# Optimization experiments

Measured on AMD Instinct MI355X. Metric: run time of the kernel, lower is better.

Reference implementation:

```python
import jax, jax.numpy as jnp
import numpy as np
from functools import partial

# Config (BranchNet 'big'-style)
HIST = [42, 78, 150, 294, 582]
PW = [3, 6, 12, 24, 48]
SHIFTING = [False, False, True, True, True]
CW = 7          # conv width
F = 32          # conv filters
E = 32          # embedding dims
B = 4096        # batch
H_TOT = 590     # total history length
V = 8192        # 2**(pc_hash_bits+1)
WBITS = 2       # weight quantization bits
ABITS = 3       # activation quantization bits
EPS = 1e-5


@partial(jax.custom_vjp, nondiff_argnums=(1,))
def quant_signed(x, bits):
    # Quantize.forward (signed, bits>1): round(x*scale)/scale, scale=(1<<(bits-1))-1
    scale = float((1 << (bits - 1)) - 1)
    return jnp.round(x * scale) / scale

def _q_fwd(x, bits):
    return quant_signed(x, bits), None

def _q_bwd(bits, res, g):
    # straight-through estimator, matching Quantize.backward
    return (g,)

quant_signed.defvjp(_q_fwd, _q_bwd)


def batchnorm(x, gamma, beta, axes, pshape):
    # training-mode BatchNorm1d: batch statistics, biased variance
    m = jnp.mean(x, axis=axes, keepdims=True)
    v = jnp.var(x, axis=axes, keepdims=True)
    return gamma.reshape(pshape) * (x - m) * jax.lax.rsqrt(v + EPS) + beta.reshape(pshape)


def extract_slice_history(x, global_shift, slice_size, pooling_width, shifting):
    # vectorized version of the per-sample Python loop in extract_slice_history
    h_tot = x.shape[1]
    if shifting:
        s = jnp.mod(global_shift, pooling_width)              # [B]
        start = (h_tot - s - slice_size)[:, None]             # [B,1]
        idx = start + jnp.arange(slice_size)[None, :]         # [B,L]
        return jnp.take_along_axis(x, idx, axis=1)
    return x[:, -slice_size:]


def fc_layer(x, W, b, gamma, beta):
    # FCLayer with quantized weights + batchnorm + hardtanh + quantized act
    w = quant_signed(jnp.clip(W, -1.0, 1.0), WBITS)
    y = x @ w.T + b
    y = batchnorm(y, gamma, beta, (0,), (1, -1))
    y = jnp.clip(y, -1.0, 1.0)  # hardtanh
    return quant_signed(y, ABITS)


def branchnet_forward(x, global_shift, emb, conv_w, conv_b, bn1_g, bn1_b,
                      bnp_g, bnp_b, W1, b1, g1, be1, W2, b2, g2, be2, W3, b3):
    feats = []
    for i in range(len(HIST)):
        L, pw = HIST[i], PW[i]
        xs = extract_slice_history(x, global_shift, L, pw, SHIFTING[i])  # [B,L] int
        e = jnp.take(emb[i], xs, axis=0)                                 # [B,L,E]
        e = jnp.transpose(e, (0, 2, 1))                                  # [B,E,L]
        h = jax.lax.conv_general_dilated(
            e, conv_w[i], window_strides=(1,), padding='VALID',
            dimension_numbers=('NCH', 'OIH', 'NCH')) + conv_b[i][None, :, None]
        h = batchnorm(h, bn1_g[i], bn1_b[i], (0, 2), (1, -1, 1))
        h = jnp.tanh(h)
        T = (L - CW + 1) // pw                                           # = 12
        p = h[:, :, :T * pw].reshape(h.shape[0], F, T, pw).mean(axis=-1) # AvgPool1d
        p = batchnorm(p, bnp_g[i], bnp_b[i], (0, 2), (1, -1, 1))
        feats.append(p.reshape(p.shape[0], -1))                          # [B, F*T]
    z = jnp.concatenate(feats, axis=1)                                   # [B, 1920]
    z = fc_layer(z, W1, b1, g1, be1)
    z = fc_layer(z, W2, b2, g2, be2)
    w3 = quant_signed(jnp.clip(W3, -1.0, 1.0), WBITS)
    out = z @ w3.T + b3                                                  # [B,1]
    return out[:, 0]                                                     # squeeze(dim=1)


def setup_inputs() -> dict:
    key = jax.random.key(0)
    ks = jax.random.split(key, 12)
    return {
        'x': jax.random.randint(ks[0], (B, H_TOT), 0, V, dtype=jnp.int32),
        'global_shift': jax.random.randint(ks[1], (B,), 0, 48, dtype=jnp.int32),
        'emb': jax.random.normal(ks[2], (5, V, E), jnp.float32) * 0.1,
        'conv_w': jax.random.normal(ks[3], (5, F, E, CW), jnp.float32) * 0.1,
        'conv_b': jax.random.normal(ks[4], (5, F), jnp.float32) * 0.01,
        'bn1_g': jnp.ones((5, F), jnp.float32),
        'bn1_b': jnp.zeros((5, F), jnp.float32),
        'bnp_g': jnp.ones((5, F), jnp.float32),
        'bnp_b': jnp.zeros((5, F), jnp.float32),
        'W1': jax.random.uniform(ks[5], (2048, 1920), jnp.float32, -1.0, 1.0),
        'b1': jax.random.normal(ks[6], (2048,), jnp.float32) * 0.01,
        'g1': jnp.ones((2048,), jnp.float32),
        'be1': jnp.zeros((2048,), jnp.float32),
        'W2': jax.random.uniform(ks[7], (2048, 2048), jnp.float32, -1.0, 1.0),
        'b2': jax.random.normal(ks[8], (2048,), jnp.float32) * 0.01,
        'g2': jnp.ones((2048,), jnp.float32),
        'be2': jnp.zeros((2048,), jnp.float32),
        'W3': jax.random.uniform(ks[9], (1, 2048), jnp.float32, -1.0, 1.0),
        'b3': jax.random.normal(ks[10], (1,), jnp.float32) * 0.01,
    }


def reference(x, global_shift, emb, conv_w, conv_b, bn1_g, bn1_b, bnp_g, bnp_b,
              W1, b1, g1, be1, W2, b2, g2, be2, W3, b3):
    return branchnet_forward(x, global_shift, emb, conv_w, conv_b, bn1_g, bn1_b,
                             bnp_g, bnp_b, W1, b1, g1, be1, W2, b2, g2, be2, W3, b3)
```

## Files before the change

kernel.cpp:

```cpp
#include <hip/hip_runtime.h>
#include <cmath>

#define HTOT  590
#define BATCH 4096
#define VOCAB 8192

typedef _Float16 f16;
typedef __attribute__((ext_vector_type(8))) _Float16 f16x8;
typedef __attribute__((ext_vector_type(4))) _Float16 f16x4;
typedef __attribute__((ext_vector_type(4))) float f32x4;
typedef __attribute__((ext_vector_type(16))) float f32x16;

constexpr size_t OFF_EHL  = 0;
constexpr size_t OFF_WF   = 1310720;
constexpr size_t OFF_PA   = 1347584;
constexpr size_t OFF_PB   = 2921472;
constexpr size_t OFF_BN1  = 4494336;
constexpr size_t OFF_BNP  = 4494656;
constexpr size_t OFF_CP   = 4494976;
constexpr size_t OFF_BNF1 = 4626048;
constexpr size_t OFF_PRAW = 4630528;
constexpr size_t OFF_W1P  = 12494848;
constexpr size_t OFF_W2P  = 14460928;
constexpr size_t OFF_Y    = 16558080;
constexpr size_t OFF_BNF2 = 24946688;
constexpr size_t OFF_Z2K  = 0;
constexpr size_t OFF_Z3K  = 4194304;

__device__ __forceinline__ float qw(float w) {
  return rintf(fminf(fmaxf(w, -1.f), 1.f));
}
__device__ __forceinline__ float4 ld4(const float* p) {
  return *reinterpret_cast<const float4*>(p);
}
__device__ __forceinline__ float tanh_c(float u) {
  const float e = __expf(2.f*u);
  return 1.f - __fdividef(2.f, e + 1.f);
}

#define MF(A,B,C) __builtin_amdgcn_mfma_f32_32x32x16_f16(A,B,C,0,0,0)

__global__ __launch_bounds__(256) void k_eprep(const float* __restrict__ emb,
                                               f16* __restrict__ ehl)
{
  const int idx = blockIdx.x*256 + threadIdx.x;
  const int c = idx & 31, v = (idx >> 5) & 8191, slice = idx >> 18;
  const float val = emb[(size_t)(slice*VOCAB + v)*32 + c];
  const f16 hi = (f16)val;
  const f16 lo = (f16)((val - (float)hi)*2048.f);
  f16* row = ehl + (size_t)(slice*VOCAB + v)*64;
  row[c] = hi; row[32 + c] = lo;
}

__global__ __launch_bounds__(256) void k_wfprep(const float* __restrict__ convw,
                                                f16* __restrict__ wf)
{
  const int idx = blockIdx.x*256 + threadIdx.x;
  const int j = idx & 7, lane = (idx >> 3) & 63, hl = (idx >> 9) & 1, ks = (idx >> 10) & 1;
  const int kk = idx >> 11, k = kk % 7, slice = kk / 7;
  const int f = lane & 31, c = ks*16 + (lane >> 5)*8 + j;
  const float val = convw[((slice*32 + f)*32 + c)*7 + k];
  const f16 hi = (f16)val;
  wf[idx] = hl ? (f16)((val - (float)hi)*2048.f) : hi;
}

template<int PASS>
__global__ __launch_bounds__(256, 2) void k_convm(const int* __restrict__ x,
                                                  const int* __restrict__ gshift,
                                                  const float* __restrict__ ehl,
                                                  const float* __restrict__ wfrag,
                                                  const float* __restrict__ bn1,
                                                  float* __restrict__ z,
                                                  float* __restrict__ partials)
{
  const int b = blockIdx.x;
  const int type = blockIdx.y;
  const int tid = threadIdx.x;
  const int wid = tid >> 6, lane = tid & 63;
  const int lt = lane & 31, hf = lane >> 5;

  __shared__ float smem[10584];
  __shared__ int   tokid[294];
  __shared__ float stat[(PASS==0)?256:4];

  float* tokrow = smem;
  float* thbuf  = smem;
  float* poolb  = smem + 4224;

  const int gsv = gshift[b];
  const int NTOK = (type == 0) ? 270 : 294;

  for (int i = tid; i < NTOK; i += 256) {
    int xs, q = i;
    if (type == 0) {
      if (i < 42)       { xs = 548; }
      else if (i < 120) { xs = 512; q = i - 42; }
      else              { xs = 440 - gsv % 12; q = i - 120; }
    } else if (type == 1) xs = 296 - gsv % 24;
    else if (type == 2)   xs = 8 - gsv % 48;
    else                  xs = 8 - gsv % 48 + 288;
    int xi = xs + q; if (xi < 0) xi += HTOT;
    tokid[i] = x[b*HTOT + xi];
  }
  __syncthreads();

  for (int j = tid; j < NTOK*8; j += 256) {
    const int row = j >> 3, ch = j & 7;
    const int sl = (type == 0) ? (row < 42 ? 0 : (row < 120 ? 1 : 2)) : ((type == 1) ? 3 : 4);
    const float4 v = ld4(ehl + (size_t)(sl*VOCAB + tokid[row])*32 + ch*4);
    *reinterpret_cast<float4*>(&tokrow[row*36 + ch*4]) = v;
  }
  __syncthreads();

  int slice, tb, nt, slotoff, ThV, pw, si;
  if (type == 0) {
    if      (wid == 0) { slice=0; tb=0;  nt=2; slotoff=0;   ThV=36;  pw=3;  si=0; }
    else if (wid == 1) { slice=1; tb=0;  nt=3; slotoff=42;  ThV=72;  pw=6;  si=1; }
    else if (wid == 2) { slice=2; tb=0;  nt=3; slotoff=120; ThV=144; pw=12; si=2; }
    else               { slice=2; tb=96; nt=2; slotoff=120; ThV=144; pw=12; si=2; }
  } else if (type == 1) {
    slice=3; pw=24; ThV=288; slotoff=0; si=0;
    tb = (wid == 0) ? 0 : 32 + wid*64; nt = (wid == 0) ? 3 : 2;
  } else if (type == 2) {
    slice=4; pw=48; ThV=288; slotoff=0; si=0;
    tb = (wid == 0) ? 0 : 32 + wid*64; nt = (wid == 0) ? 3 : 2;
  } else {
    slice=4; pw=48; ThV=576; slotoff=-288; si=0;
    tb = 288 + ((wid == 0) ? 0 : 32 + wid*64); nt = (wid == 0) ? 3 : 2;
  }
  const int wb = (type == 3) ? 6 : 0;

  const float* wfsl = wfrag + slice*7168;
  #define LDA(K,KS,HL) (*reinterpret_cast<const f16x8*>(wfsl + (((K)*2+(KS))*2+(HL))*256 + lane*4))

  f32x16 a0[3], a1[3];
  #pragma unroll
  for (int r = 0; r < 3; ++r) {
    #pragma unroll
    for (int i = 0; i < 16; ++i) { a0[r][i] = 0.f; a1[r][i] = 0.f; }
  }

  const float* p0 = tokrow + (size_t)(slotoff + tb + lt)*36 + hf*4;
  const float* p1 = p0 + 1152;
  const float* p2 = p0 + 2304;
  f16x8 wh0 = LDA(0,0,0), wl0 = LDA(0,0,1), wh1 = LDA(0,1,0), wl1 = LDA(0,1,1);
  #pragma unroll 1
  for (int k = 0; k < 7; ++k) {
    f16x8 nh0, nl0, nh1, nl1;
    if (k < 6) { nh0 = LDA(k+1,0,0); nl0 = LDA(k+1,0,1); nh1 = LDA(k+1,1,0); nl1 = LDA(k+1,1,1); }
    {
      const f16x8 bh0 = *(const f16x8*)(p0),    bh1 = *(const f16x8*)(p0+8);
      const f16x8 bl0 = *(const f16x8*)(p0+16), bl1 = *(const f16x8*)(p0+24);
      a0[0]=MF(wh0,bh0,a0[0]); a1[0]=MF(wh0,bl0,a1[0]); a1[0]=MF(wl0,bh0,a1[0]);
      a0[0]=MF(wh1,bh1,a0[0]); a1[0]=MF(wh1,bl1,a1[0]); a1[0]=MF(wl1,bh1,a1[0]);
    }
    if (nt > 1) {
      const f16x8 bh0 = *(const f16x8*)(p1),    bh1 = *(const f16x8*)(p1+8);
      const f16x8 bl0 = *(const f16x8*)(p1+16), bl1 = *(const f16x8*)(p1+24);
      a0[1]=MF(wh0,bh0,a0[1]); a1[1]=MF(wh0,bl0,a1[1]); a1[1]=MF(wl0,bh0,a1[1]);
      a0[1]=MF(wh1,bh1,a0[1]); a1[1]=MF(wh1,bl1,a1[1]); a1[1]=MF(wl1,bh1,a1[1]);
    }
    if (nt > 2) {
      const f16x8 bh0 = *(const f16x8*)(p2),    bh1 = *(const f16x8*)(p2+8);
      const f16x8 bl0 = *(const f16x8*)(p2+16), bl1 = *(const f16x8*)(p2+24);
      a0[2]=MF(wh0,bh0,a0[2]); a1[2]=MF(wh0,bl0,a1[2]); a1[2]=MF(wl0,bh0,a1[2]);
      a0[2]=MF(wh1,bh1,a0[2]); a1[2]=MF(wh1,bl1,a1[2]); a1[2]=MF(wl1,bh1,a1[2]);
    }
    p0 += 36; p1 += 36; p2 += 36;
    wh0 = nh0; wl0 = nl0; wh1 = nh1; wl1 = nl1;
  }
  __syncthreads();

  if (PASS == 1) {
    for (int i = tid; i < 2304; i += 256) poolb[i] = 0.f;
  }
  __syncthreads();

  float sv1[16], sv2[16], A1v[16], B1v[16];
  if (PASS == 0) {
    #pragma unroll
    for (int i = 0; i < 16; ++i) { sv1[i] = 0.f; sv2[i] = 0.f; }
  } else {
    #pragma unroll
    for (int i = 0; i < 16; ++i) {
      const int fr = (i&3) + 8*(i>>2) + 4*hf;
      A1v[i] = bn1[slice*32 + fr];
      B1v[i] = bn1[160 + slice*32 + fr];
    }
  }

  #pragma unroll
  for (int r = 0; r < 3; ++r) if (r < nt) {
    const int tbg = tb + r*32;
    float h[16];
    #pragma unroll
    for (int i = 0; i < 16; ++i) h[i] = a0[r][i] + a1[r][i]*(1.f/2048.f);
    if (PASS == 0) {
      const bool tv = (tbg + lt) < ThV;
      #pragma unroll
      for (int i = 0; i < 16; ++i) {
        const float hv = tv ? h[i] : 0.f;
        sv1[i] += hv; sv2[i] += hv*hv;
      }
    } else {
      #pragma unroll
      for (int i = 0; i < 16; ++i) {
        const int fr = (i&3) + 8*(i>>2) + 4*hf;
        thbuf[wid*1056 + fr*33 + lt] = tanh_c(A1v[i]*h[i] + B1v[i]);
      }
      const int tvend = min(tbg + 32, ThV);
      const int wlo = tbg / pw, whi = (tvend - 1) / pw;
      for (int w = wlo; w <= whi; ++w) {
        const int lo = max(w*pw, tbg), hi2 = min((w+1)*pw, tvend);
        float s = 0.f;
        for (int t = lo + hf; t < hi2; t += 2) s += thbuf[wid*1056 + lt*33 + (t - tbg)];
        s += __shfl_xor(s, 32);
        if (hf == 0) {
          const int piece = (w*pw < tbg) ? 1 : 0;
          poolb[(si*12 + (w - wb))*64 + piece*32 + lt] = s;
        }
      }
    }
  }

  if (PASS == 0) {
    #pragma unroll
    for (int i = 0; i < 16; ++i) {
      #pragma unroll
      for (int m = 1; m < 32; m <<= 1) {
        sv1[i] += __shfl_xor(sv1[i], m, 32);
        sv2[i] += __shfl_xor(sv2[i], m, 32);
      }
    }
    if (lt == 0) {
      #pragma unroll
      for (int i = 0; i < 16; ++i) {
        stat[wid*64 + hf*32 + i*2]     = sv1[i];
        stat[wid*64 + hf*32 + i*2 + 1] = sv2[i];
      }
    }
  }
  __syncthreads();

  const int nch = (type == 0) ? 96 : 32;
  if (tid < nch) {
    const int sic = tid >> 5, f = tid & 31;
    const int sg = (type == 0) ? sic : ((type == 1) ? 3 : 4);
    const int P = (sg < 4) ? sg*32 + f : ((type == 2) ? 128 + f : 160 + f);
    float s1 = 0.f, s2 = 0.f;
    if (PASS == 0) {
      const int hfc = (f >> 2) & 1, ic = (f & 3) + 4*(f >> 3);
      #pragma unroll
      for (int w = 0; w < 4; ++w) {
        const int wsi = (type == 0) ? ((w < 2) ? w : 2) : 0;
        if (wsi == sic) {
          s1 += stat[w*64 + hfc*32 + ic*2];
          s2 += stat[w*64 + hfc*32 + ic*2 + 1];
        }
      }
    } else {
      const int pwc = (type == 0) ? ((sic == 0) ? 3 : (sic == 1) ? 6 : 12)
                                  : ((type == 1) ? 24 : 48);
      const int nwin = (type >= 2) ? 6 : 12;
      const int wbc = (type == 3) ? 6 : 0;
      const float inv = 1.f/(float)pwc;
      for (int wl = 0; wl < nwin; ++wl) {
        const float p = (poolb[(sic*12 + wl)*64 + f] + poolb[(sic*12 + wl)*64 + 32 + f]) * inv;
        z[(size_t)b*1920 + sg*384 + (wl + wbc)*32 + f] = p;
        s1 += p; s2 += p*p;
      }
    }
    partials[(size_t)b*384 + P*2]     = s1;
    partials[(size_t)b*384 + P*2 + 1] = s2;
  }
}

template<int PASS>
__global__ __launch_bounds__(256) void k_bnfinal(const float* __restrict__ partials,
                                                 const float* __restrict__ gamma,
                                                 const float* __restrict__ beta,
                                                 float* __restrict__ outAB)
{
  const int c = blockIdx.x;
  const int slice = c >> 5, f = c & 31;
  const int tid = threadIdx.x;
  double s1 = 0.0, s2 = 0.0;
  for (int b = tid; b < BATCH; b += 256) {
    const float* p = partials + (size_t)b*384;
    if (slice < 4) { s1 += p[(slice*32+f)*2]; s2 += p[(slice*32+f)*2+1]; }
    else {
      s1 += (double)p[(128+f)*2]   + (double)p[(160+f)*2];
      s2 += (double)p[(128+f)*2+1] + (double)p[(160+f)*2+1];
    }
  }
  __shared__ double r1[256], r2[256];
  r1[tid] = s1; r2[tid] = s2;
  __syncthreads();
  for (int off = 128; off > 0; off >>= 1) {
    if (tid < off) { r1[tid] += r1[tid+off]; r2[tid] += r2[tid+off]; }
    __syncthreads();
  }
  if (tid == 0) {
    long N;
    if (PASS == 0) { const long Tall[5] = {36,72,144,288,576}; N = (long)BATCH * Tall[slice]; }
    else           { N = (long)BATCH * 12; }
    const double m   = r1[0]/(double)N;
    const double var = r2[0]/(double)N - m*m;
    const float rstd = (float)(1.0/sqrt(var + 1e-5));
    const float Aa = gamma[c]*rstd;
    outAB[c]       = Aa;
    outAB[160 + c] = beta[c] - Aa*(float)m;
  }
}

__global__ __launch_bounds__(256) void k_znorm(float* __restrict__ zz,
                                               const float* __restrict__ bnp)
{
  const size_t i4 = (size_t)blockIdx.x*256 + threadIdx.x;
  const float4 v = ld4(zz + i4*4);
  const int j = (int)((i4*4) % 1920);
  const int slice = j / 384, f0 = j & 31;
  const float4 A = ld4(bnp + slice*32 + f0);
  const float4 B = ld4(bnp + 160 + slice*32 + f0);
  const float zn[4] = {v.x*A.x+B.x, v.y*A.y+B.y, v.z*A.z+B.z, v.w*A.w+B.w};
  uint4 pk;
  unsigned w[4];
  #pragma unroll
  for (int e = 0; e < 4; ++e) {
    const f16 hi = (f16)zn[e];
    const f16 lo = (f16)(zn[e] - (float)hi);
    w[e] = (unsigned)__builtin_bit_cast(unsigned short, hi)
         | ((unsigned)__builtin_bit_cast(unsigned short, lo) << 16);
  }
  pk.x = w[0]; pk.y = w[1]; pk.z = w[2]; pk.w = w[3];
  *reinterpret_cast<uint4*>(zz + i4*4) = pk;
}

__global__ __launch_bounds__(256) void k_wprep1(const float* __restrict__ W1,
                                                f16* __restrict__ W1p)
{
  const int idx = blockIdx.x*256 + threadIdx.x;
  const int n = idx / 1920, klds = idx - n*1920;
  const int slice = klds / 384, r = klds - slice*384;
  const int tp = r >> 5, f = r & 31;
  W1p[idx] = (f16)qw(W1[n*1920 + slice*384 + f*12 + tp]);
}

__global__ __launch_bounds__(256) void k_wprep2(const float* __restrict__ W2,
                                                f16* __restrict__ W2p)
{
  const size_t i4 = (size_t)blockIdx.x*256 + threadIdx.x;
  const float4 v = ld4(W2 + i4*4);
  f16x4 o;
  o[0] = (f16)qw(v.x); o[1] = (f16)qw(v.y); o[2] = (f16)qw(v.z); o[3] = (f16)qw(v.w);
  *reinterpret_cast<f16x4*>(&W2p[i4*4]) = o;
}

template<int SPLIT, int PACKED>
__global__ __launch_bounds__(256) void k_mfgemm(const f16* __restrict__ Ahi,
                                               const unsigned* __restrict__ Apk,
                                               const f16* __restrict__ Bp,
                                               float* __restrict__ C,
                                               const int K, const float oscale)
{
  __shared__ f16 sA[(SPLIT+1)*128][40];
  __shared__ f16 sB[128][40];
  const int tid = threadIdx.x;
  const int bm = blockIdx.y*128, bn = blockIdx.x*128;
  const int wid = tid >> 6, lane = tid & 63;
  const int wm = (wid >> 1)*64, wn = (wid & 1)*64;
  const int lgrp = lane >> 4, lrow = lane & 15;
  f32x4 acc[4][4];
  #pragma unroll
  for (int m = 0; m < 4; ++m)
    #pragma unroll
    for (int n = 0; n < 4; ++n) acc[m][n] = (f32x4){0.f,0.f,0.f,0.f};

  const int srow = tid >> 2, sc = (tid & 3)*8;
  for (int k0 = 0; k0 < K; k0 += 32) {
    #pragma unroll
    for (int u = 0; u < 2; ++u) {
      const int row = srow + u*64;
      if (PACKED) {
        const unsigned* ap = Apk + (size_t)(bm+row)*K + k0 + sc;
        const uint4 v0 = *reinterpret_cast<const uint4*>(ap);
        const uint4 v1 = *reinterpret_cast<const uint4*>(ap + 4);
        uint4 hi, lo;
        hi.x = (v0.x & 0xffffu) | (v0.y << 16);  hi.y = (v0.z & 0xffffu) | (v0.w << 16);
        hi.z = (v1.x & 0xffffu) | (v1.y << 16);  hi.w = (v1.z & 0xffffu) | (v1.w << 16);
        lo.x = (v0.x >> 16) | (v0.y & 0xffff0000u);  lo.y = (v0.z >> 16) | (v0.w & 0xffff0000u);
        lo.z = (v1.x >> 16) | (v1.y & 0xffff0000u);  lo.w = (v1.z >> 16) | (v1.w & 0xffff0000u);
        *reinterpret_cast<uint4*>(&sA[row][sc])     = hi;
        *reinterpret_cast<uint4*>(&sA[128+row][sc]) = lo;
      } else {
        const uint4 va = *reinterpret_cast<const uint4*>(&Ahi[(size_t)(bm+row)*K + k0 + sc]);
        *reinterpret_cast<uint4*>(&sA[row][sc]) = va;
      }
      const uint4 vb = *reinterpret_cast<const uint4*>(&Bp[(size_t)(bn+row)*K + k0 + sc]);
      *reinterpret_cast<uint4*>(&sB[row][sc]) = vb;
    }
    __syncthreads();
    f16x8 bf[4];
    #pragma unroll
    for (int n = 0; n < 4; ++n)
      bf[n] = *reinterpret_cast<const f16x8*>(&sB[wn + n*16 + lrow][lgrp*8]);
    #pragma unroll
    for (int m = 0; m < 4; ++m) {
      const f16x8 ah = *reinterpret_cast<const f16x8*>(&sA[wm + m*16 + lrow][lgrp*8]);
      #pragma unroll
      for (int n = 0; n < 4; ++n)
        acc[m][n] = __builtin_amdgcn_mfma_f32_16x16x32_f16(ah, bf[n], acc[m][n], 0, 0, 0);
      if (SPLIT) {
        const f16x8 al = *reinterpret_cast<const f16x8*>(&sA[128 + wm + m*16 + lrow][lgrp*8]);
        #pragma unroll
        for (int n = 0; n < 4; ++n)
          acc[m][n] = __builtin_amdgcn_mfma_f32_16x16x32_f16(al, bf[n], acc[m][n], 0, 0, 0);
      }
    }
    __syncthreads();
  }
  #pragma unroll
  for (int m = 0; m < 4; ++m)
    #pragma unroll
    for (int n = 0; n < 4; ++n) {
      const int col = bn + wn + n*16 + lrow;
      #pragma unroll
      for (int r = 0; r < 4; ++r)
        C[(size_t)(bm + wm + m*16 + lgrp*4 + r)*2048 + col] = acc[m][n][r]*oscale;
    }
}

__global__ __launch_bounds__(256) void k_colpart(const float* __restrict__ Y,
                                                 double* __restrict__ part, int N)
{
  const int c0 = blockIdx.x*64;
  const int chunk = blockIdx.y;
  const int tid = threadIdx.x;
  const int c = tid & 63, rq = tid >> 6;
  double s1 = 0.0, s2 = 0.0;
  const int rbase = chunk*256;
  for (int r = rbase + rq; r < rbase+256; r += 4) {
    const float v = Y[(size_t)r*N + c0 + c];
    s1 += (double)v; s2 += (double)v*(double)v;
  }
  __shared__ double r1[256], r2[256];
  r1[tid] = s1; r2[tid] = s2;
  __syncthreads();
  if (tid < 64) {
    const double a  = r1[tid]+r1[tid+64]+r1[tid+128]+r1[tid+192];
    const double cc = r2[tid]+r2[tid+64]+r2[tid+128]+r2[tid+192];
    part[(size_t)(c0+c)*32 + chunk*2]     = a;
    part[(size_t)(c0+c)*32 + chunk*2 + 1] = cc;
  }
}

__global__ __launch_bounds__(256) void k_colfinal(const double* __restrict__ part,
                                                  const float* __restrict__ gamma,
                                                  const float* __restrict__ beta,
                                                  float* __restrict__ bnfc, int N)
{
  const int c = blockIdx.x*256 + threadIdx.x;
  if (c >= N) return;
  double s1 = 0.0, s2 = 0.0;
  #pragma unroll
  for (int ch = 0; ch < 16; ++ch) {
    s1 += part[(size_t)c*32 + ch*2];
    s2 += part[(size_t)c*32 + ch*2 + 1];
  }
  const double m   = s1/4096.0;
  const double var = s2/4096.0 - m*m;
  const float rstd = (float)(1.0/sqrt(var + 1e-5));
  const float Aa = gamma[c]*rstd;
  bnfc[c]        = Aa;
  bnfc[2048 + c] = beta[c] - Aa*(float)m;
}

__global__ __launch_bounds__(256) void k_act(const float* __restrict__ Y,
                                             const float* __restrict__ bnfc,
                                             f16* __restrict__ Zk)
{
  const size_t i4 = (size_t)blockIdx.x*256 + threadIdx.x;
  const int cbase = (int)((i4*4) & 2047);
  const float4 v = ld4(Y + i4*4);
  const float4 A = ld4(bnfc + cbase);
  const float4 B = ld4(bnfc + 2048 + cbase);
  const float t[4] = {v.x*A.x+B.x, v.y*A.y+B.y, v.z*A.z+B.z, v.w*A.w+B.w};
  f16x4 o;
  #pragma unroll
  for (int e = 0; e < 4; ++e) {
    const float c = fminf(fmaxf(t[e], -1.f), 1.f);
    o[e] = (f16)rintf(c*3.f);
  }
  *reinterpret_cast<f16x4*>(&Zk[i4*4]) = o;
}

__global__ __launch_bounds__(256) void k_final(const f16* __restrict__ Z3,
                                               const float* __restrict__ W3,
                                               const float* __restrict__ b3,
                                               float* __restrict__ out)
{
  const int b = blockIdx.x;
  const int tid = threadIdx.x;
  float s = 0.f;
  for (int j = tid; j < 2048; j += 256)
    s += (float)Z3[(size_t)b*2048 + j] * qw(W3[j]);
  __shared__ float red[256];
  red[tid] = s;
  __syncthreads();
  for (int off = 128; off > 0; off >>= 1) {
    if (tid < off) red[tid] += red[tid+off];
    __syncthreads();
  }
  if (tid == 0) out[b] = red[0]*(1.f/3.f) + b3[0];
}

extern "C" void kernel_launch(void* const* d_in, const int* in_sizes, int n_in,
                              void* d_out, int out_size, void* d_ws, size_t ws_size,
                              hipStream_t stream)
{
  const int*   x    = (const int*)d_in[0];
  const int*   gs   = (const int*)d_in[1];
  const float* emb  = (const float*)d_in[2];
  const float* cw   = (const float*)d_in[3];
  const float* bn1g = (const float*)d_in[5];
  const float* bn1b = (const float*)d_in[6];
  const float* bnpg = (const float*)d_in[7];
  const float* bnpb = (const float*)d_in[8];
  const float* W1   = (const float*)d_in[9];
  const float* g1   = (const float*)d_in[11];
  const float* be1  = (const float*)d_in[12];
  const float* W2   = (const float*)d_in[13];
  const float* g2   = (const float*)d_in[15];
  const float* be2  = (const float*)d_in[16];
  const float* W3   = (const float*)d_in[17];
  const float* b3   = (const float*)d_in[18];
  float* ws  = (float*)d_ws;
  float* out = (float*)d_out;

  k_eprep<<<5120, 256, 0, stream>>>(emb, (f16*)(ws + OFF_EHL));
  k_wfprep<<<280, 256, 0, stream>>>(cw, (f16*)(ws + OFF_WF));

  k_convm<0><<<dim3(BATCH, 4), 256, 0, stream>>>(x, gs, ws + OFF_EHL, ws + OFF_WF,
                                                 ws + OFF_BN1, nullptr, ws + OFF_PA);
  k_bnfinal<0><<<160, 256, 0, stream>>>(ws + OFF_PA, bn1g, bn1b, ws + OFF_BN1);
  k_convm<1><<<dim3(BATCH, 4), 256, 0, stream>>>(x, gs, ws + OFF_EHL, ws + OFF_WF,
                                                 ws + OFF_BN1, ws + OFF_PRAW, ws + OFF_PB);
  k_bnfinal<1><<<160, 256, 0, stream>>>(ws + OFF_PB, bnpg, bnpb, ws + OFF_BNP);
  k_znorm<<<7680, 256, 0, stream>>>(ws + OFF_PRAW, ws + OFF_BNP);
  k_wprep1<<<15360, 256, 0, stream>>>(W1, (f16*)(ws + OFF_W1P));
  k_wprep2<<<4096, 256, 0, stream>>>(W2, (f16*)(ws + OFF_W2P));

  k_mfgemm<1,1><<<dim3(16, 32), 256, 0, stream>>>(nullptr, (const unsigned*)(ws + OFF_PRAW),
                                                  (const f16*)(ws + OFF_W1P),
                                                  ws + OFF_Y, 1920, 1.f);
  k_colpart<<<dim3(32, 16), 256, 0, stream>>>(ws + OFF_Y, (double*)(ws + OFF_CP), 2048);
  k_colfinal<<<8, 256, 0, stream>>>((const double*)(ws + OFF_CP), g1, be1, ws + OFF_BNF1, 2048);
  k_act<<<8192, 256, 0, stream>>>(ws + OFF_Y, ws + OFF_BNF1, (f16*)(ws + OFF_Z2K));

  k_mfgemm<0,0><<<dim3(16, 32), 256, 0, stream>>>((const f16*)(ws + OFF_Z2K), nullptr,
                                                  (const f16*)(ws + OFF_W2P),
                                                  ws + OFF_Y, 2048, 1.f/3.f);
  k_colpart<<<dim3(32, 16), 256, 0, stream>>>(ws + OFF_Y, (double*)(ws + OFF_CP), 2048);
  k_colfinal<<<8, 256, 0, stream>>>((const double*)(ws + OFF_CP), g2, be2, ws + OFF_BNF2, 2048);
  k_act<<<8192, 256, 0, stream>>>(ws + OFF_Y, ws + OFF_BNF2, (f16*)(ws + OFF_Z3K));

  k_final<<<4096, 256, 0, stream>>>((const f16*)(ws + OFF_Z3K), W3, b3, out);
}
```

Baseline: 886.4 us.

## Split conv work into eight smaller blocks per sample to cut LDS and registers

The conv kernel now launches 8 block types per sample instead of 4. Each block covers at most 150 tokens with one or two 32-position tiles per wave instead of up to three, so LDS use is about halved and the stat buffer is aliased into shared memory. The min-blocks launch bound is removed, weight-fragment prefetch across k is dropped, and the partials layout and BN-final reduction are extended to more pieces. This aims to raise occupancy and balance work, at the cost of more blocks, repeated gathers and setup per block, and less latency hiding inside each block.

New measurement: 1.247 ms. 40.7% more time.

```diff
diff --git a/kernel.cpp b/kernel.cpp
--- a/kernel.cpp
+++ b/kernel.cpp
@@ -13,17 +13,17 @@
 
 constexpr size_t OFF_EHL  = 0;
 constexpr size_t OFF_WF   = 1310720;
-constexpr size_t OFF_PA   = 1347584;
-constexpr size_t OFF_PB   = 2921472;
-constexpr size_t OFF_BN1  = 4494336;
-constexpr size_t OFF_BNP  = 4494656;
-constexpr size_t OFF_CP   = 4494976;
-constexpr size_t OFF_BNF1 = 4626048;
-constexpr size_t OFF_PRAW = 4630528;
-constexpr size_t OFF_W1P  = 12494848;
-constexpr size_t OFF_W2P  = 14460928;
-constexpr size_t OFF_Y    = 16558080;
-constexpr size_t OFF_BNF2 = 24946688;
+constexpr size_t OFF_PA   = 1346560;
+constexpr size_t OFF_PB   = 3705856;
+constexpr size_t OFF_BN1  = 6065152;
+constexpr size_t OFF_BNP  = 6065472;
+constexpr size_t OFF_CP   = 6065792;
+constexpr size_t OFF_BNF1 = 6196864;
+constexpr size_t OFF_PRAW = 6200960;
+constexpr size_t OFF_W1P  = 14065280;
+constexpr size_t OFF_W2P  = 16031360;
+constexpr size_t OFF_Y    = 18128512;
+constexpr size_t OFF_BNF2 = 26517120;
 constexpr size_t OFF_Z2K  = 0;
 constexpr size_t OFF_Z3K  = 4194304;
 
@@ -65,13 +65,13 @@
 }
 
 template<int PASS>
-__global__ __launch_bounds__(256, 2) void k_convm(const int* __restrict__ x,
-                                                  const int* __restrict__ gshift,
-                                                  const float* __restrict__ ehl,
-                                                  const float* __restrict__ wfrag,
-                                                  const float* __restrict__ bn1,
-                                                  float* __restrict__ z,
-                                                  float* __restrict__ partials)
+__global__ __launch_bounds__(256) void k_convm(const int* __restrict__ x,
+                                               const int* __restrict__ gshift,
+                                               const float* __restrict__ ehl,
+                                               const float* __restrict__ wfrag,
+                                               const float* __restrict__ bn1,
+                                               float* __restrict__ z,
+                                               float* __restrict__ partials)
 {
   const int b = blockIdx.x;
   const int type = blockIdx.y;
@@ -79,75 +79,67 @@
   const int wid = tid >> 6, lane = tid & 63;
   const int lt = lane & 31, hf = lane >> 5;
 
-  __shared__ float smem[10584];
-  __shared__ int   tokid[294];
-  __shared__ float stat[(PASS==0)?256:4];
+  __shared__ float smem[5976];
+  __shared__ int   tokid[150];
 
   float* tokrow = smem;
   float* thbuf  = smem;
   float* poolb  = smem + 4224;
+  float* stat   = smem;
 
   const int gsv = gshift[b];
-  const int NTOK = (type == 0) ? 270 : 294;
+  const int NTOK = (type == 0) ? 120 : 150;
+
+  int xbase = 0;
+  if      (type == 1) xbase = 440 - gsv % 12;
+  else if (type == 2) xbase = 296 - gsv % 24;
+  else if (type == 3) xbase = 296 - gsv % 24 + 144;
+  else if (type >= 4) xbase = 8 - gsv % 48 + (type - 4)*144;
 
   for (int i = tid; i < NTOK; i += 256) {
-    int xs, q = i;
-    if (type == 0) {
-      if (i < 42)       { xs = 548; }
-      else if (i < 120) { xs = 512; q = i - 42; }
-      else              { xs = 440 - gsv % 12; q = i - 120; }
-    } else if (type == 1) xs = 296 - gsv % 24;
-    else if (type == 2)   xs = 8 - gsv % 48;
-    else                  xs = 8 - gsv % 48 + 288;
-    int xi = xs + q; if (xi < 0) xi += HTOT;
+    int xi;
+    if (type == 0) xi = (i < 42) ? (548 + i) : (512 + (i - 42));
+    else { xi = xbase + i; if (xi < 0) xi += HTOT; }
     tokid[i] = x[b*HTOT + xi];
   }
   __syncthreads();
 
+  const int esl = (type == 0) ? 0 : ((type == 1) ? 2 : ((type <= 3) ? 3 : 4));
   for (int j = tid; j < NTOK*8; j += 256) {
     const int row = j >> 3, ch = j & 7;
-    const int sl = (type == 0) ? (row < 42 ? 0 : (row < 120 ? 1 : 2)) : ((type == 1) ? 3 : 4);
+    const int sl = (type == 0) ? (row < 42 ? 0 : 1) : esl;
     const float4 v = ld4(ehl + (size_t)(sl*VOCAB + tokid[row])*32 + ch*4);
     *reinterpret_cast<float4*>(&tokrow[row*36 + ch*4]) = v;
   }
   __syncthreads();
 
-  int slice, tb, nt, slotoff, ThV, pw, si;
+  int slice, slotoff, tb, nt, ThV, pw, si;
   if (type == 0) {
-    if      (wid == 0) { slice=0; tb=0;  nt=2; slotoff=0;   ThV=36;  pw=3;  si=0; }
-    else if (wid == 1) { slice=1; tb=0;  nt=3; slotoff=42;  ThV=72;  pw=6;  si=1; }
-    else if (wid == 2) { slice=2; tb=0;  nt=3; slotoff=120; ThV=144; pw=12; si=2; }
-    else               { slice=2; tb=96; nt=2; slotoff=120; ThV=144; pw=12; si=2; }
-  } else if (type == 1) {
-    slice=3; pw=24; ThV=288; slotoff=0; si=0;
-    tb = (wid == 0) ? 0 : 32 + wid*64; nt = (wid == 0) ? 3 : 2;
-  } else if (type == 2) {
-    slice=4; pw=48; ThV=288; slotoff=0; si=0;
-    tb = (wid == 0) ? 0 : 32 + wid*64; nt = (wid == 0) ? 3 : 2;
+    if (wid == 0) { slice=0; slotoff=0;  tb=0;           nt=2; ThV=36; pw=3; si=0; }
+    else          { slice=1; slotoff=42; tb=(wid-1)*32;  nt=1; ThV=72; pw=6; si=1; }
   } else {
-    slice=4; pw=48; ThV=576; slotoff=-288; si=0;
-    tb = 288 + ((wid == 0) ? 0 : 32 + wid*64); nt = (wid == 0) ? 3 : 2;
-  }
-  const int wb = (type == 3) ? 6 : 0;
+    slice = (type == 1) ? 2 : ((type <= 3) ? 3 : 4);
+    slotoff = 0; si = 0; ThV = 144;
+    pw = (type == 1) ? 12 : ((type <= 3) ? 24 : 48);
+    tb = (wid == 0) ? 0 : (32 + wid*32);
+    nt = (wid == 0) ? 2 : 1;
+  }
 
   const float* wfsl = wfrag + slice*7168;
   #define LDA(K,KS,HL) (*reinterpret_cast<const f16x8*>(wfsl + (((K)*2+(KS))*2+(HL))*256 + lane*4))
 
-  f32x16 a0[3], a1[3];
-  #pragma unroll
-  for (int r = 0; r < 3; ++r) {
+  f32x16 a0[2], a1[2];
+  #pragma unroll
+  for (int r = 0; r < 2; ++r) {
     #pragma unroll
     for (int i = 0; i < 16; ++i) { a0[r][i] = 0.f; a1[r][i] = 0.f; }
   }
 
   const float* p0 = tokrow + (size_t)(slotoff + tb + lt)*36 + hf*4;
-  const float* p1 = p0 + 1152;
-  const float* p2 = p0 + 2304;
-  f16x8 wh0 = LDA(0,0,0), wl0 = LDA(0,0,1), wh1 = LDA(0,1,0), wl1 = LDA(0,1,1);
+  const float* p1 = p0 + 32*36;
   #pragma unroll 1
   for (int k = 0; k < 7; ++k) {
-    f16x8 nh0, nl0, nh1, nl1;
-    if (k < 6) { nh0 = LDA(k+1,0,0); nl0 = LDA(k+1,0,1); nh1 = LDA(k+1,1,0); nl1 = LDA(k+1,1,1); }
+    const f16x8 wh0 = LDA(k,0,0), wl0 = LDA(k,0,1), wh1 = LDA(k,1,0), wl1 = LDA(k,1,1);
     {
       const f16x8 bh0 = *(const f16x8*)(p0),    bh1 = *(const f16x8*)(p0+8);
       const f16x8 bl0 = *(const f16x8*)(p0+16), bl1 = *(const f16x8*)(p0+24);
@@ -160,19 +152,12 @@
       a0[1]=MF(wh0,bh0,a0[1]); a1[1]=MF(wh0,bl0,a1[1]); a1[1]=MF(wl0,bh0,a1[1]);
       a0[1]=MF(wh1,bh1,a0[1]); a1[1]=MF(wh1,bl1,a1[1]); a1[1]=MF(wl1,bh1,a1[1]);
     }
-    if (nt > 2) {
-      const f16x8 bh0 = *(const f16x8*)(p2),    bh1 = *(const f16x8*)(p2+8);
-      const f16x8 bl0 = *(const f16x8*)(p2+16), bl1 = *(const f16x8*)(p2+24);
-      a0[2]=MF(wh0,bh0,a0[2]); a1[2]=MF(wh0,bl0,a1[2]); a1[2]=MF(wl0,bh0,a1[2]);
-      a0[2]=MF(wh1,bh1,a0[2]); a1[2]=MF(wh1,bl1,a1[2]); a1[2]=MF(wl1,bh1,a1[2]);
-    }
-    p0 += 36; p1 += 36; p2 += 36;
-    wh0 = nh0; wl0 = nl0; wh1 = nh1; wl1 = nl1;
+    p0 += 36; p1 += 36;
   }
   __syncthreads();
 
   if (PASS == 1) {
-    for (int i = tid; i < 2304; i += 256) poolb[i] = 0.f;
+    for (int i = tid; i < 1536; i += 256) poolb[i] = 0.f;
   }
   __syncthreads();
 
@@ -190,7 +175,7 @@
   }
 
   #pragma unroll
-  for (int r = 0; r < 3; ++r) if (r < nt) {
+  for (int r = 0; r < 2; ++r) if (r < nt) {
     const int tbg = tb + r*32;
     float h[16];
     #pragma unroll
@@ -217,7 +202,7 @@
         s += __shfl_xor(s, 32);
         if (hf == 0) {
           const int piece = (w*pw < tbg) ? 1 : 0;
-          poolb[(si*12 + (w - wb))*64 + piece*32 + lt] = s;
+          poolb[(si*12 + w)*64 + piece*32 + lt] = s;
         }
       }
     }
@@ -242,36 +227,37 @@
   }
   __syncthreads();
 
-  const int nch = (type == 0) ? 96 : 32;
+  const int nch = (type == 0) ? 64 : 32;
   if (tid < nch) {
     const int sic = tid >> 5, f = tid & 31;
-    const int sg = (type == 0) ? sic : ((type == 1) ? 3 : 4);
-    const int P = (sg < 4) ? sg*32 + f : ((type == 2) ? 128 + f : 160 + f);
+    int sg, Pb, wb2, nwin; float invpw;
+    if (type == 0) {
+      sg = sic; Pb = sic*32; wb2 = 0; nwin = 12;
+      invpw = (sic == 0) ? (1.f/3.f) : (1.f/6.f);
+    } else if (type == 1) { sg=2; Pb=64;  wb2=0;          nwin=12; invpw=1.f/12.f; }
+    else if   (type == 2) { sg=3; Pb=96;  wb2=0;          nwin=6;  invpw=1.f/24.f; }
+    else if   (type == 3) { sg=3; Pb=128; wb2=6;          nwin=6;  invpw=1.f/24.f; }
+    else { sg=4; Pb=160+(type-4)*32; wb2=(type-4)*3;      nwin=3;  invpw=1.f/48.f; }
     float s1 = 0.f, s2 = 0.f;
     if (PASS == 0) {
       const int hfc = (f >> 2) & 1, ic = (f & 3) + 4*(f >> 3);
       #pragma unroll
       for (int w = 0; w < 4; ++w) {
-        const int wsi = (type == 0) ? ((w < 2) ? w : 2) : 0;
+        const int wsi = (type == 0) ? ((w == 0) ? 0 : 1) : 0;
         if (wsi == sic) {
           s1 += stat[w*64 + hfc*32 + ic*2];
           s2 += stat[w*64 + hfc*32 + ic*2 + 1];
         }
       }
     } else {
-      const int pwc = (type == 0) ? ((sic == 0) ? 3 : (sic == 1) ? 6 : 12)
-                                  : ((type == 1) ? 24 : 48);
-      const int nwin = (type >= 2) ? 6 : 12;
-      const int wbc = (type == 3) ? 6 : 0;
-      const float inv = 1.f/(float)pwc;
       for (int wl = 0; wl < nwin; ++wl) {
-        const float p = (poolb[(sic*12 + wl)*64 + f] + poolb[(sic*12 + wl)*64 + 32 + f]) * inv;
-        z[(size_t)b*1920 + sg*384 + (wl + wbc)*32 + f] = p;
+        const float p = (poolb[(sic*12 + wl)*64 + f] + poolb[(sic*12 + wl)*64 + 32 + f]) * invpw;
+        z[(size_t)b*1920 + sg*384 + (wl + wb2)*32 + f] = p;
         s1 += p; s2 += p*p;
       }
     }
-    partials[(size_t)b*384 + P*2]     = s1;
-    partials[(size_t)b*384 + P*2 + 1] = s2;
+    partials[(size_t)b*576 + (Pb + f)*2]     = s1;
+    partials[(size_t)b*576 + (Pb + f)*2 + 1] = s2;
   }
 }
 
@@ -286,11 +272,17 @@
   const int tid = threadIdx.x;
   double s1 = 0.0, s2 = 0.0;
   for (int b = tid; b < BATCH; b += 256) {
-    const float* p = partials + (size_t)b*384;
-    if (slice < 4) { s1 += p[(slice*32+f)*2]; s2 += p[(slice*32+f)*2+1]; }
-    else {
-      s1 += (double)p[(128+f)*2]   + (double)p[(160+f)*2];
-      s2 += (double)p[(128+f)*2+1] + (double)p[(160+f)*2+1];
+    const float* p = partials + (size_t)b*576;
+    if (slice < 3) {
+      s1 += p[(slice*32+f)*2]; s2 += p[(slice*32+f)*2+1];
+    } else if (slice == 3) {
+      s1 += (double)p[(96+f)*2]   + (double)p[(128+f)*2];
+      s2 += (double)p[(96+f)*2+1] + (double)p[(128+f)*2+1];
+    } else {
+      s1 += (double)p[(160+f)*2]   + (double)p[(192+f)*2]
+          + (double)p[(224+f)*2]   + (double)p[(256+f)*2];
+      s2 += (double)p[(160+f)*2+1] + (double)p[(192+f)*2+1]
+          + (double)p[(224+f)*2+1] + (double)p[(256+f)*2+1];
     }
   }
   __shared__ double r1[256], r2[256];
@@ -540,10 +532,10 @@
   k_eprep<<<5120, 256, 0, stream>>>(emb, (f16*)(ws + OFF_EHL));
   k_wfprep<<<280, 256, 0, stream>>>(cw, (f16*)(ws + OFF_WF));
 
-  k_convm<0><<<dim3(BATCH, 4), 256, 0, stream>>>(x, gs, ws + OFF_EHL, ws + OFF_WF,
+  k_convm<0><<<dim3(BATCH, 8), 256, 0, stream>>>(x, gs, ws + OFF_EHL, ws + OFF_WF,
                                                  ws + OFF_BN1, nullptr, ws + OFF_PA);
   k_bnfinal<0><<<160, 256, 0, stream>>>(ws + OFF_PA, bn1g, bn1b, ws + OFF_BN1);
-  k_convm<1><<<dim3(BATCH, 4), 256, 0, stream>>>(x, gs, ws + OFF_EHL, ws + OFF_WF,
+  k_convm<1><<<dim3(BATCH, 8), 256, 0, stream>>>(x, gs, ws + OFF_EHL, ws + OFF_WF,
                                                  ws + OFF_BN1, ws + OFF_PRAW, ws + OFF_PB);
   k_bnfinal<1><<<160, 256, 0, stream>>>(ws + OFF_PB, bnpg, bnpb, ws + OFF_BNP);
   k_znorm<<<7680, 256, 0, stream>>>(ws + OFF_PRAW, ws + OFF_BNP);
```
